# Kernel tuning notes

Measured on AMD Instinct MI355X. Metric: run time of the kernel, lower is better.

Reference implementation:

```python
import jax, jax.numpy as jnp
import numpy as np

H = 1024  # hidden_size
N = 2 * H # encoder feature dim


def setup_inputs() -> dict:
    key = jax.random.key(0)
    ks = jax.random.split(key, 8)
    T, B = 2048, 16
    dec = jax.random.normal(ks[0], (B, H), dtype=jnp.float32)
    enc = jax.random.normal(ks[1], (T, B, N), dtype=jnp.float32)
    mask = jax.random.randint(ks[2], (T, B), 0, 2) > 0
    cov = jax.random.uniform(ks[3], (T, B), dtype=jnp.float32)
    # parameters (PyTorch Linear convention: y = x @ W.T + b)
    Wd = jax.random.normal(ks[4], (N, H), dtype=jnp.float32) / np.sqrt(H)
    bd = jnp.zeros((N,), dtype=jnp.float32)
    wc = jax.random.normal(ks[5], (N,), dtype=jnp.float32)  # coverage_projection: Linear(1, N, bias=False)
    v = jax.random.normal(ks[6], (N,), dtype=jnp.float32) / np.sqrt(N)  # v: Linear(N, 1, bias=False)
    return {"decoder_hidden_states": dec, "encoder_outs": enc,
            "encoder_padding_mask": mask, "coverage": cov,
            "Wd": Wd, "bd": bd, "wc": wc, "v": v}


def reference(decoder_hidden_states, encoder_outs, encoder_padding_mask, coverage, Wd, bd, wc, v):
    # dec_fea: [B, N]
    dec_fea = decoder_hidden_states @ Wd.T + bd
    # att_features: [T, B, N] = enc + broadcast dec + coverage feature
    att = encoder_outs + dec_fea[None, :, :] + coverage[:, :, None] * wc[None, None, :]
    e = jnp.tanh(att)
    # attn_scores: [T, B] via matvec with v
    scores = jnp.einsum('tbn,n->tb', e, v)
    scores = jnp.where(encoder_padding_mask, -jnp.inf, scores)
    attn_dist = jax.nn.softmax(scores, axis=0)  # softmax over T
    # context: [B, N]
    c = jnp.einsum('tb,tbn->bn', attn_dist, encoder_outs)
    coverage_out = coverage + attn_dist
    return (c, attn_dist, coverage_out)
```

## Files before the change

kernel.cpp:

```cpp
#include <hip/hip_runtime.h>


#define HH 1024
#define NNF 2048
#define TTT 2048
#define BB 16
#define NCHUNK 64
#define ROWS 32

#define WS_DECFEA 0
#define WS_P      (BB * NNF)
#define WS_LPART  (WS_P + TTT * BB)
#define WS_LINV   (WS_LPART + NCHUNK * BB)
#define WS_CPART  (WS_LINV + 16)

__device__ __forceinline__ float tanh_fast(float x) {
    float e = __expf(2.0f * x);
    return 1.0f - 2.0f * __builtin_amdgcn_rcpf(e + 1.0f);
}

__global__ __launch_bounds__(256) void k_decfea(const float* __restrict__ dec,
                                                const float* __restrict__ Wd,
                                                const float* __restrict__ bd,
                                                float* __restrict__ dec_fea) {
    int gw   = (blockIdx.x * 256 + threadIdx.x) >> 6;
    int lane = threadIdx.x & 63;
    int b = gw >> 11;
    int n = gw & (NNF - 1);
    const float* dr = dec + b * HH;
    const float* wr = Wd + (size_t)n * HH;
    float acc = 0.0f;
#pragma unroll
    for (int it = 0; it < 4; ++it) {
        int h = it * 256 + lane * 4;
        float4 a = *(const float4*)(dr + h);
        float4 w = *(const float4*)(wr + h);
        acc = fmaf(a.x, w.x, acc);
        acc = fmaf(a.y, w.y, acc);
        acc = fmaf(a.z, w.z, acc);
        acc = fmaf(a.w, w.w, acc);
    }
#pragma unroll
    for (int off = 32; off; off >>= 1) acc += __shfl_down(acc, off, 64);
    if (lane == 0) dec_fea[b * NNF + n] = acc + bd[n];
}

__global__ __launch_bounds__(256) void k_main(const float* __restrict__ enc,
                                              const int* __restrict__ mask,
                                              const float* __restrict__ cov,
                                              const float* __restrict__ wc,
                                              const float* __restrict__ v,
                                              float* __restrict__ ws) {
    const int b     = blockIdx.y;
    const int chunk = blockIdx.x;
    const int t0    = chunk * ROWS;
    const int tid   = threadIdx.x;
    const int lane  = tid & 63;
    const int wid   = tid >> 6;
    const int n0    = tid * 4;
    const int n1    = 1024 + tid * 4;

    const float* dec_fea = ws + WS_DECFEA;
    float* ws_p     = ws + WS_P;
    float* ws_lpart = ws + WS_LPART;
    float* cpart    = ws + WS_CPART;

    const float4 d0 = *(const float4*)(dec_fea + b * NNF + n0);
    const float4 d1 = *(const float4*)(dec_fea + b * NNF + n1);
    const float4 w0 = *(const float4*)(wc + n0);
    const float4 w1 = *(const float4*)(wc + n1);
    const float4 v0 = *(const float4*)(v + n0);
    const float4 v1 = *(const float4*)(v + n1);

    float4 c0 = {0.f, 0.f, 0.f, 0.f};
    float4 c1 = {0.f, 0.f, 0.f, 0.f};
    float l_loc = 0.0f;

    __shared__ float red[2][4];

    const float* base = enc + ((size_t)t0 * BB + b) * NNF;
    float4 e0 = *(const float4*)(base + n0);
    float4 e1 = *(const float4*)(base + n1);

    for (int r = 0; r < ROWS; ++r) {
        const int t = t0 + r;
        float4 f0 = e0, f1 = e1;
        if (r + 1 < ROWS) {
            const float* nb = base + (size_t)(r + 1) * BB * NNF;
            e0 = *(const float4*)(nb + n0);
            e1 = *(const float4*)(nb + n1);
        }
        const float cv = cov[t * BB + b];

        float s = 0.0f;
        {
            float a;
            a = fmaf(cv, w0.x, f0.x + d0.x); s = fmaf(tanh_fast(a), v0.x, s);
            a = fmaf(cv, w0.y, f0.y + d0.y); s = fmaf(tanh_fast(a), v0.y, s);
            a = fmaf(cv, w0.z, f0.z + d0.z); s = fmaf(tanh_fast(a), v0.z, s);
            a = fmaf(cv, w0.w, f0.w + d0.w); s = fmaf(tanh_fast(a), v0.w, s);
            a = fmaf(cv, w1.x, f1.x + d1.x); s = fmaf(tanh_fast(a), v1.x, s);
            a = fmaf(cv, w1.y, f1.y + d1.y); s = fmaf(tanh_fast(a), v1.y, s);
            a = fmaf(cv, w1.z, f1.z + d1.z); s = fmaf(tanh_fast(a), v1.z, s);
            a = fmaf(cv, w1.w, f1.w + d1.w); s = fmaf(tanh_fast(a), v1.w, s);
        }
#pragma unroll
        for (int off = 32; off; off >>= 1) s += __shfl_down(s, off, 64);
        if (lane == 0) red[r & 1][wid] = s;
        __syncthreads();
        const float stot = red[r & 1][0] + red[r & 1][1] + red[r & 1][2] + red[r & 1][3];

        const bool pad = mask[t * BB + b] != 0;
        const float p = pad ? 0.0f : __expf(stot);

        c0.x = fmaf(p, f0.x, c0.x);
        c0.y = fmaf(p, f0.y, c0.y);
        c0.z = fmaf(p, f0.z, c0.z);
        c0.w = fmaf(p, f0.w, c0.w);
        c1.x = fmaf(p, f1.x, c1.x);
        c1.y = fmaf(p, f1.y, c1.y);
        c1.z = fmaf(p, f1.z, c1.z);
        c1.w = fmaf(p, f1.w, c1.w);

        if (tid == 0) {
            ws_p[t * BB + b] = p;
            l_loc += p;
        }
    }

    if (tid == 0) ws_lpart[chunk * BB + b] = l_loc;
    float* cp = cpart + (size_t)(chunk * BB + b) * NNF;
    *(float4*)(cp + n0) = c0;
    *(float4*)(cp + n1) = c1;
}

__global__ void k_linv(float* __restrict__ ws) {
    int b = threadIdx.x;
    if (b < BB) {
        float s = 0.0f;
        for (int j = 0; j < NCHUNK; ++j) s += ws[WS_LPART + j * BB + b];
        ws[WS_LINV + b] = 1.0f / s;
    }
}

__global__ __launch_bounds__(256) void k_finc(const float* __restrict__ ws,
                                              float* __restrict__ out_c) {
    int gid  = blockIdx.x * 256 + threadIdx.x;
    int idx4 = gid * 4;
    int b = idx4 >> 11;
    int n = idx4 & (NNF - 1);
    float4 s = {0.f, 0.f, 0.f, 0.f};
    for (int j = 0; j < NCHUNK; ++j) {
        float4 a = *(const float4*)(ws + WS_CPART + (size_t)(j * BB + b) * NNF + n);
        s.x += a.x; s.y += a.y; s.z += a.z; s.w += a.w;
    }
    float li = ws[WS_LINV + b];
    s.x *= li; s.y *= li; s.z *= li; s.w *= li;
    *(float4*)(out_c + idx4) = s;
}

__global__ __launch_bounds__(256) void k_fina(const float* __restrict__ ws,
                                              const float* __restrict__ cov,
                                              float* __restrict__ out_attn,
                                              float* __restrict__ out_cov) {
    int idx = blockIdx.x * 256 + threadIdx.x;
    int b = idx & (BB - 1);
    float a = ws[WS_P + idx] * ws[WS_LINV + b];
    out_attn[idx] = a;
    out_cov[idx] = cov[idx] + a;
}

extern "C" void kernel_launch(void* const* d_in, const int* in_sizes, int n_in,
                              void* d_out, int out_size, void* d_ws, size_t ws_size,
                              hipStream_t stream) {
    const float* dec  = (const float*)d_in[0];
    const float* enc  = (const float*)d_in[1];
    const int*   mask = (const int*)d_in[2];
    const float* cov  = (const float*)d_in[3];
    const float* Wd   = (const float*)d_in[4];
    const float* bd   = (const float*)d_in[5];
    const float* wc   = (const float*)d_in[6];
    const float* v    = (const float*)d_in[7];
    float* ws  = (float*)d_ws;
    float* out = (float*)d_out;

    float* out_c    = out;
    float* out_attn = out + BB * NNF;
    float* out_cov  = out_attn + TTT * BB;

    k_decfea<<<8192, 256, 0, stream>>>(dec, Wd, bd, ws + WS_DECFEA);

    dim3 g2(NCHUNK, BB);
    k_main<<<g2, 256, 0, stream>>>(enc, mask, cov, wc, v, ws);

    k_linv<<<1, 64, 0, stream>>>(ws);

    k_finc<<<32, 256, 0, stream>>>(ws, out_c);

    k_fina<<<128, 256, 0, stream>>>(ws, cov, out_attn, out_cov);
}
```

Measured before the change: 393.3 us.

## Give each wavefront whole rows in k_main and merge finalize kernels

The main kernel now assigns each wavefront 8 full time rows, 2048 features each. This replaces the per-row block-wide reduction and __syncthreads with a wave-local xor-shuffle reduction, and the next row is double-buffered in registers. Partial contexts from the four waves are combined through shared memory before being written out. The three finalize kernels (linv, context, attn/coverage) are merged into one launch that recomputes the normalizers per block. Register use rises sharply (several float4[8] arrays per thread), which may reduce occupancy.

```diff
diff --git a/kernel.cpp b/kernel.cpp
--- a/kernel.cpp
+++ b/kernel.cpp
@@ -6,7 +6,6 @@
 #define TTT 2048
 #define BB 16
 #define NCHUNK 64
-#define ROWS 32
 
 #define WS_DECFEA 0
 #define WS_P      (BB * NNF)
@@ -45,6 +44,38 @@
     if (lane == 0) dec_fea[b * NNF + n] = acc + bd[n];
 }
 
+
+__device__ __forceinline__ void load_row8(const float* __restrict__ p, int nb,
+                                          float4* dst) {
+#pragma unroll
+    for (int j = 0; j < 8; ++j) dst[j] = *(const float4*)(p + j * 256 + nb);
+}
+
+__device__ __forceinline__ float score8(const float4* e, const float4* d,
+                                        const float4* w, const float4* vv,
+                                        float cv) {
+    float s = 0.0f;
+#pragma unroll
+    for (int j = 0; j < 8; ++j) {
+        float a;
+        a = fmaf(cv, w[j].x, e[j].x + d[j].x); s = fmaf(tanh_fast(a), vv[j].x, s);
+        a = fmaf(cv, w[j].y, e[j].y + d[j].y); s = fmaf(tanh_fast(a), vv[j].y, s);
+        a = fmaf(cv, w[j].z, e[j].z + d[j].z); s = fmaf(tanh_fast(a), vv[j].z, s);
+        a = fmaf(cv, w[j].w, e[j].w + d[j].w); s = fmaf(tanh_fast(a), vv[j].w, s);
+    }
+    return s;
+}
+
+__device__ __forceinline__ void acc8(float4* acc, const float4* e, float p) {
+#pragma unroll
+    for (int j = 0; j < 8; ++j) {
+        acc[j].x = fmaf(p, e[j].x, acc[j].x);
+        acc[j].y = fmaf(p, e[j].y, acc[j].y);
+        acc[j].z = fmaf(p, e[j].z, acc[j].z);
+        acc[j].w = fmaf(p, e[j].w, acc[j].w);
+    }
+}
+
 __global__ __launch_bounds__(256) void k_main(const float* __restrict__ enc,
                                               const int* __restrict__ mask,
                                               const float* __restrict__ cov,
@@ -53,121 +84,135 @@
                                               float* __restrict__ ws) {
     const int b     = blockIdx.y;
     const int chunk = blockIdx.x;
-    const int t0    = chunk * ROWS;
     const int tid   = threadIdx.x;
     const int lane  = tid & 63;
     const int wid   = tid >> 6;
-    const int n0    = tid * 4;
-    const int n1    = 1024 + tid * 4;
+    const int t0    = chunk * 32 + wid * 8;
+    const int nb    = lane * 4;
 
     const float* dec_fea = ws + WS_DECFEA;
     float* ws_p     = ws + WS_P;
     float* ws_lpart = ws + WS_LPART;
     float* cpart    = ws + WS_CPART;
 
-    const float4 d0 = *(const float4*)(dec_fea + b * NNF + n0);
-    const float4 d1 = *(const float4*)(dec_fea + b * NNF + n1);
-    const float4 w0 = *(const float4*)(wc + n0);
-    const float4 w1 = *(const float4*)(wc + n1);
-    const float4 v0 = *(const float4*)(v + n0);
-    const float4 v1 = *(const float4*)(v + n1);
-
-    float4 c0 = {0.f, 0.f, 0.f, 0.f};
-    float4 c1 = {0.f, 0.f, 0.f, 0.f};
+    float4 dfr[8], wcr[8], vfr[8];
+#pragma unroll
+    for (int j = 0; j < 8; ++j) {
+        dfr[j] = *(const float4*)(dec_fea + b * NNF + j * 256 + nb);
+        wcr[j] = *(const float4*)(wc + j * 256 + nb);
+        vfr[j] = *(const float4*)(v + j * 256 + nb);
+    }
+
+    float cv_r[8];
+    int mkbits = 0;
+#pragma unroll
+    for (int r = 0; r < 8; ++r) {
+        cv_r[r] = cov[(t0 + r) * BB + b];
+        mkbits |= (mask[(t0 + r) * BB + b] != 0) << r;
+    }
+
+    const float* base = enc + ((size_t)t0 * BB + b) * NNF;
+    const size_t rstride = (size_t)BB * NNF;
+
+    float4 bufA[8], bufB[8];
+    load_row8(base, nb, bufA);
+
+    float4 acc[8];
+#pragma unroll
+    for (int j = 0; j < 8; ++j) acc[j] = make_float4(0.f, 0.f, 0.f, 0.f);
     float l_loc = 0.0f;
 
-    __shared__ float red[2][4];
-
-    const float* base = enc + ((size_t)t0 * BB + b) * NNF;
-    float4 e0 = *(const float4*)(base + n0);
-    float4 e1 = *(const float4*)(base + n1);
-
-    for (int r = 0; r < ROWS; ++r) {
-        const int t = t0 + r;
-        float4 f0 = e0, f1 = e1;
-        if (r + 1 < ROWS) {
-            const float* nb = base + (size_t)(r + 1) * BB * NNF;
-            e0 = *(const float4*)(nb + n0);
-            e1 = *(const float4*)(nb + n1);
+#pragma unroll
+    for (int rr = 0; rr < 4; ++rr) {
+        const int r0 = 2 * rr, r1 = 2 * rr + 1;
+
+        load_row8(base + (size_t)r1 * rstride, nb, bufB);
+        {
+            float s = score8(bufA, dfr, wcr, vfr, cv_r[r0]);
+#pragma unroll
+            for (int off = 1; off < 64; off <<= 1) s += __shfl_xor(s, off, 64);
+            const float p = ((mkbits >> r0) & 1) ? 0.0f : __expf(s);
+            l_loc += p;
+            if (lane == 0) ws_p[(t0 + r0) * BB + b] = p;
+            acc8(acc, bufA, p);
         }
-        const float cv = cov[t * BB + b];
-
-        float s = 0.0f;
+
+        if (rr < 3) load_row8(base + (size_t)(r1 + 1) * rstride, nb, bufA);
         {
-            float a;
-            a = fmaf(cv, w0.x, f0.x + d0.x); s = fmaf(tanh_fast(a), v0.x, s);
-            a = fmaf(cv, w0.y, f0.y + d0.y); s = fmaf(tanh_fast(a), v0.y, s);
-            a = fmaf(cv, w0.z, f0.z + d0.z); s = fmaf(tanh_fast(a), v0.z, s);
-            a = fmaf(cv, w0.w, f0.w + d0.w); s = fmaf(tanh_fast(a), v0.w, s);
-            a = fmaf(cv, w1.x, f1.x + d1.x); s = fmaf(tanh_fast(a), v1.x, s);
-            a = fmaf(cv, w1.y, f1.y + d1.y); s = fmaf(tanh_fast(a), v1.y, s);
-            a = fmaf(cv, w1.z, f1.z + d1.z); s = fmaf(tanh_fast(a), v1.z, s);
-            a = fmaf(cv, w1.w, f1.w + d1.w); s = fmaf(tanh_fast(a), v1.w, s);
+            float s = score8(bufB, dfr, wcr, vfr, cv_r[r1]);
+#pragma unroll
+            for (int off = 1; off < 64; off <<= 1) s += __shfl_xor(s, off, 64);
+            const float p = ((mkbits >> r1) & 1) ? 0.0f : __expf(s);
+            l_loc += p;
+            if (lane == 0) ws_p[(t0 + r1) * BB + b] = p;
+            acc8(acc, bufB, p);
         }
-#pragma unroll
-        for (int off = 32; off; off >>= 1) s += __shfl_down(s, off, 64);
-        if (lane == 0) red[r & 1][wid] = s;
-        __syncthreads();
-        const float stot = red[r & 1][0] + red[r & 1][1] + red[r & 1][2] + red[r & 1][3];
-
-        const bool pad = mask[t * BB + b] != 0;
-        const float p = pad ? 0.0f : __expf(stot);
-
-        c0.x = fmaf(p, f0.x, c0.x);
-        c0.y = fmaf(p, f0.y, c0.y);
-        c0.z = fmaf(p, f0.z, c0.z);
-        c0.w = fmaf(p, f0.w, c0.w);
-        c1.x = fmaf(p, f1.x, c1.x);
-        c1.y = fmaf(p, f1.y, c1.y);
-        c1.z = fmaf(p, f1.z, c1.z);
-        c1.w = fmaf(p, f1.w, c1.w);
-
-        if (tid == 0) {
-            ws_p[t * BB + b] = p;
-            l_loc += p;
+    }
+
+    __shared__ float4 smc[4][512];
+    __shared__ float  sml[4];
+#pragma unroll
+    for (int j = 0; j < 8; ++j) smc[wid][j * 64 + lane] = acc[j];
+    if (lane == 0) sml[wid] = l_loc;
+    __syncthreads();
+    if (tid == 0) ws_lpart[chunk * BB + b] = (sml[0] + sml[1]) + (sml[2] + sml[3]);
+    float* cp = cpart + (size_t)(chunk * BB + b) * NNF;
+#pragma unroll
+    for (int i = tid; i < 512; i += 256) {
+        float4 s0 = smc[0][i], s1 = smc[1][i], s2 = smc[2][i], s3 = smc[3][i];
+        float4 o;
+        o.x = (s0.x + s1.x) + (s2.x + s3.x);
+        o.y = (s0.y + s1.y) + (s2.y + s3.y);
+        o.z = (s0.z + s1.z) + (s2.z + s3.z);
+        o.w = (s0.w + s1.w) + (s2.w + s3.w);
+        const int j = i >> 6, l = i & 63;
+        *(float4*)(cp + j * 256 + l * 4) = o;
+    }
+}
+
+__global__ __launch_bounds__(256) void k_final(const float* __restrict__ ws,
+                                               const float* __restrict__ cov,
+                                               float* __restrict__ out_c,
+                                               float* __restrict__ out_attn,
+                                               float* __restrict__ out_cov) {
+    const int tid = threadIdx.x;
+    const int bx  = blockIdx.x;
+
+    __shared__ float sm[16][16];
+    __shared__ float linv_s[16];
+    const float* lp = ws + WS_LPART;
+    float s4 = (lp[tid] + lp[tid + 256]) + (lp[tid + 512] + lp[tid + 768]);
+    sm[tid >> 4][tid & 15] = s4;
+    __syncthreads();
+    if (tid < 16) {
+        float t = 0.0f;
+#pragma unroll
+        for (int k = 0; k < 16; ++k) t += sm[k][tid];
+        linv_s[tid] = 1.0f / t;
+    }
+    __syncthreads();
+
+    if (bx < 32) {
+        const int idx4 = (bx * 256 + tid) * 4;
+        const int b = idx4 >> 11;
+        const int n = idx4 & (NNF - 1);
+        const float* cp = ws + WS_CPART + (size_t)b * NNF + n;
+        float4 s = make_float4(0.f, 0.f, 0.f, 0.f);
+#pragma unroll 8
+        for (int j = 0; j < NCHUNK; ++j) {
+            float4 a = *(const float4*)(cp + (size_t)j * BB * NNF);
+            s.x += a.x; s.y += a.y; s.z += a.z; s.w += a.w;
         }
-    }
-
-    if (tid == 0) ws_lpart[chunk * BB + b] = l_loc;
-    float* cp = cpart + (size_t)(chunk * BB + b) * NNF;
-    *(float4*)(cp + n0) = c0;
-    *(float4*)(cp + n1) = c1;
-}
-
-__global__ void k_linv(float* __restrict__ ws) {
-    int b = threadIdx.x;
-    if (b < BB) {
-        float s = 0.0f;
-        for (int j = 0; j < NCHUNK; ++j) s += ws[WS_LPART + j * BB + b];
-        ws[WS_LINV + b] = 1.0f / s;
-    }
-}
-
-__global__ __launch_bounds__(256) void k_finc(const float* __restrict__ ws,
-                                              float* __restrict__ out_c) {
-    int gid  = blockIdx.x * 256 + threadIdx.x;
-    int idx4 = gid * 4;
-    int b = idx4 >> 11;
-    int n = idx4 & (NNF - 1);
-    float4 s = {0.f, 0.f, 0.f, 0.f};
-    for (int j = 0; j < NCHUNK; ++j) {
-        float4 a = *(const float4*)(ws + WS_CPART + (size_t)(j * BB + b) * NNF + n);
-        s.x += a.x; s.y += a.y; s.z += a.z; s.w += a.w;
-    }
-    float li = ws[WS_LINV + b];
-    s.x *= li; s.y *= li; s.z *= li; s.w *= li;
-    *(float4*)(out_c + idx4) = s;
-}
-
-__global__ __launch_bounds__(256) void k_fina(const float* __restrict__ ws,
-                                              const float* __restrict__ cov,
-                                              float* __restrict__ out_attn,
-                                              float* __restrict__ out_cov) {
-    int idx = blockIdx.x * 256 + threadIdx.x;
-    int b = idx & (BB - 1);
-    float a = ws[WS_P + idx] * ws[WS_LINV + b];
-    out_attn[idx] = a;
-    out_cov[idx] = cov[idx] + a;
+        const float li = linv_s[b];
+        s.x *= li; s.y *= li; s.z *= li; s.w *= li;
+        *(float4*)(out_c + idx4) = s;
+    } else {
+        const int idx = (bx - 32) * 256 + tid;
+        const int b = idx & (BB - 1);
+        const float a = ws[WS_P + idx] * linv_s[b];
+        out_attn[idx] = a;
+        out_cov[idx] = cov[idx] + a;
+    }
 }
 
 extern "C" void kernel_launch(void* const* d_in, const int* in_sizes, int n_in,
@@ -193,9 +238,5 @@
     dim3 g2(NCHUNK, BB);
     k_main<<<g2, 256, 0, stream>>>(enc, mask, cov, wc, v, ws);
 
-    k_linv<<<1, 64, 0, stream>>>(ws);
-
-    k_finc<<<32, 256, 0, stream>>>(ws, out_c);
-
-    k_fina<<<128, 256, 0, stream>>>(ws, cov, out_attn, out_cov);
-}
+    k_final<<<160, 256, 0, stream>>>(ws, cov, out_c, out_attn, out_cov);
+}
```

Measured after the change: 396.7 us. Within noise of the previous version (+0.9%).
